# Performance work log

Measured on AMD Instinct MI355X. Metric: run time of the kernel, lower is better.

## Reference

```python
import jax, jax.numpy as jnp
import numpy as np

# --- constants (structural / non-tensor args of run()) ---
B = 1024        # number of independent systems (replicas)
NDOF = 64       # degrees of freedom per system (x0.shape[-1])
N_CHAIN = 2     # thermostat chain length
DT = 0.002      # integration time step
N_STEPS = 200   # number of MD steps


def force_fn(x):
    # harmonic potential U = 0.5*|x|^2  ->  F = -x
    return -x


def setup_inputs() -> dict:
    key = jax.random.key(0)
    k1, k2 = jax.random.split(key)
    x0 = jax.random.normal(k1, (B, NDOF), dtype=jnp.float32)
    v0 = jax.random.normal(k2, (B, NDOF), dtype=jnp.float32)
    kT = jnp.ones((), dtype=jnp.float32)
    mass = jnp.ones((), dtype=jnp.float32)
    Q = jnp.ones((), dtype=jnp.float32)
    return {"x0": x0, "v0": v0, "kT": kT, "mass": mass, "Q": Q}


def _nhc_step(x, v, xi, kT, mass, Q):
    dt = DT
    ndof = NDOF
    # xi: (..., N_CHAIN)
    KE = 0.5 * mass * jnp.sum(v * v, axis=-1)            # (...,)
    G = (2.0 * KE - ndof * kT) / Q
    xi_list = [xi[..., j] for j in range(N_CHAIN)]
    # first half chain update, j = n_chain-1 .. 0 (staggered half steps)
    for j in range(N_CHAIN - 1, -1, -1):
        if j == N_CHAIN - 1:
            xi_list[j] = xi_list[j] + dt / 4 * G
        else:
            s = jnp.exp(-xi_list[j + 1] * dt / 8)
            xi_list[j] = (xi_list[j] * s + dt / 4 * G) * s
        if j == 0:
            v = v * jnp.exp(-xi_list[0][..., None] * dt / 2)
            KE = 0.5 * mass * jnp.sum(v * v, axis=-1)
        G = (2.0 * KE - ndof * kT) / Q if j == 0 else (Q * xi_list[j - 1] ** 2 - kT) / Q
    # velocity-Verlet inner step
    v = v + dt / 2 * force_fn(x) / mass
    x = x + dt * v
    v = v + dt / 2 * force_fn(x) / mass
    KE = 0.5 * mass * jnp.sum(v * v, axis=-1)
    G = (2.0 * KE - ndof * kT) / Q
    # second half chain update, j = 0 .. n_chain-1
    for j in range(N_CHAIN):
        if j == 0:
            v = v * jnp.exp(-xi_list[0][..., None] * dt / 2)
            KE = 0.5 * mass * jnp.sum(v * v, axis=-1)
            G = (2.0 * KE - ndof * kT) / Q
        if j == N_CHAIN - 1:
            xi_list[j] = xi_list[j] + dt / 4 * G
        else:
            s = jnp.exp(-xi_list[j + 1] * dt / 8)
            xi_list[j] = (xi_list[j] * s + dt / 4 * G) * s
        G = (Q * xi_list[j] ** 2 - kT) / Q
    return x, v, jnp.stack(xi_list, axis=-1)


def _run(x0, v0, kT, mass, Q):
    xi0 = jnp.zeros(x0.shape[:-1] + (N_CHAIN,), dtype=x0.dtype)

    def body(carry, _):
        x, v, xi = carry
        x, v, xi = _nhc_step(x, v, xi, kT, mass, Q)
        return (x, v, xi), (x, v)

    _, (xs, vs) = jax.lax.scan(body, (x0, v0, xi0), xs=None, length=N_STEPS)
    traj_x = jnp.concatenate([x0[None], xs], axis=0)   # (N_STEPS+1, B, NDOF)
    traj_v = jnp.concatenate([v0[None], vs], axis=0)
    return traj_x, traj_v


def reference(x0, v0, kT, mass, Q):
    return _run(x0, v0, kT, mass, Q)
```

## Files before the change

### kernel.cpp

```cpp
#include <hip/hip_runtime.h>

#define NB     1024
#define NDOF   64
#define NSTEPS 200
#define DTF    0.002f

__global__ __launch_bounds__(256) void nhc_kernel(
    const float* __restrict__ x0, const float* __restrict__ v0,
    const float* __restrict__ kTp, const float* __restrict__ massp,
    const float* __restrict__ Qp, float* __restrict__ out)
{
    const int tid  = blockIdx.x * blockDim.x + threadIdx.x;
    const int sys  = tid >> 6;
    const int lane = tid & 63;
    if (sys >= NB) return;

    const float kT   = kTp[0];
    const float mass = massp[0];
    const float Q    = Qp[0];

    const float dt   = DTF;
    const float dt2  = 0.5f   * DTF;
    const float dt4  = 0.25f  * DTF;
    const float dt8  = 0.125f * DTF;
    const float invQ = 1.0f / Q;
    const float mi   = mass * invQ;
    const float c    = dt2 / mass;
    const float alpha = 1.0f - dt * c;

    const float K1 = c * c * (alpha + 1.0f) * (alpha + 1.0f);
    const float K2 = 2.0f * dt * c * c * (alpha + 2.0f) - 4.0f * c;
    const float K3 = alpha * alpha;
    const float A1 = alpha * alpha, A2 = 2.0f * dt * alpha, A3 = dt * dt;
    const float L1 = -c * alpha * (alpha + 1.0f);
    const float L2 = 1.0f - 2.0f * dt * c * (alpha + 1.0f);
    const float L3 = dt * alpha;
    const float Bs = -dt8, As = 0.5f * dt8 * dt8;
    const float Bc = -dt2, Ac = 0.5f * dt2 * dt2;
    const float Bu = -dt,  Au = 0.5f * dt * dt;
    const float negC   = -(float)NDOF * kT * invQ;
    const float negkTQ = -kT * invQ;

    float x = x0[sys * NDOF + lane];
    float v = v0[sys * NDOF + lane];

    float* __restrict__ out_x = out;
    float* __restrict__ out_v = out + (size_t)(NSTEPS + 1) * NB * NDOF;

    out_x[sys * NDOF + lane] = x;
    out_v[sys * NDOF + lane] = v;

    float sxx = x * x, sxv = x * v, svv = v * v;
    #pragma unroll
    for (int off = 32; off; off >>= 1) {
        sxx += __shfl_xor(sxx, off, 64);
        sxv += __shfl_xor(sxv, off, 64);
        svv += __shfl_xor(svv, off, 64);
    }
    float Sxx = mi * sxx, Sxv = mi * sxv, Svv = mi * svv;
    float P1 = K1 * Sxx, P2 = K2 * Sxv, P3 = K3 * Svv;

    float xi0 = 0.0f;
    float xi1 = dt4 * (Svv + negC);
    float t0  = dt4 * negkTQ;

    size_t widx = (size_t)NB * NDOF + sys * NDOF + lane;

    for (int n = 0; n < NSTEPS; ++n) {
        float s  = fmaf(xi1, fmaf(As, xi1, Bs), 1.0f);
        xi0 = fmaf(xi0, s, t0) * s;
        float sc = fmaf(xi0, fmaf(Ac, xi0, Bc), 1.0f);
        float u  = fmaf(xi0, fmaf(Au, xi0, Bu), 1.0f);
        float b  = fmaf(u, P3, fmaf(sc, P2, P1));
        float Gt = fmaf(u, b, negC);
        float t  = dt4 * Gt;
        xi0 = fmaf(xi0, s, t) * s;
        float G1 = fmaf(xi0, xi0, negkTQ);
        xi1 = xi1 + fmaf(dt4, G1, t);
        t0  = dt4 * G1;

        float X = sc * Sxv, V = u * Svv;
        float Sxx1 = fmaf(A1, Sxx, fmaf(A2, X, A3 * V));
        Sxv = sc * fmaf(L1, Sxx, fmaf(L2, X, L3 * V));
        Svv = u * b;
        Sxx = Sxx1;
        P1 = K1 * Sxx; P2 = K2 * Sxv; P3 = K3 * Svv;

        v *= sc;
        v = fmaf(-c, x, v);
        x = fmaf(dt, v, x);
        v = fmaf(-c, x, v);
        v *= sc;

        out_x[widx] = x;
        out_v[widx] = v;
        widx += (size_t)NB * NDOF;
    }
}

extern "C" void kernel_launch(void* const* d_in, const int* in_sizes, int n_in,
                              void* d_out, int out_size, void* d_ws, size_t ws_size,
                              hipStream_t stream) {
    const float* x0   = (const float*)d_in[0];
    const float* v0   = (const float*)d_in[1];
    const float* kT   = (const float*)d_in[2];
    const float* mass = (const float*)d_in[3];
    const float* Q    = (const float*)d_in[4];
    float* out = (float*)d_out;

    const int total = NB * NDOF;
    const int block = 256;
    const int grid  = total / block;
    nhc_kernel<<<grid, block, 0, stream>>>(x0, v0, kT, mass, Q, out);
}
```

Before: 122.2 us.

## Split NHC integration into per-step propagator scan and parallel trajectory expansion

Phase 1 runs the serial thermostat recurrence per system and accumulates a 2x2 linear propagator matrix per step, storing one float4 per (system, step) in workspace. Phase 2 launches one thread per float4 of output across all steps and computes x,v directly from x0,v0 and that matrix, giving fully parallel, vectorised, coalesced trajectory writes. The aim is to break the serial 200-step store chain of the original kernel into a bandwidth-bound parallel write. It adds a second launch, a workspace round trip, and a fallback fused kernel, and it may change rounding relative to stepwise integration.

```diff
diff --git a/kernel.cpp b/kernel.cpp
--- a/kernel.cpp
+++ b/kernel.cpp
@@ -5,10 +5,10 @@
 #define NSTEPS 200
 #define DTF    0.002f
 
-__global__ __launch_bounds__(256) void nhc_kernel(
+__global__ __launch_bounds__(256) void nhc_phase1(
     const float* __restrict__ x0, const float* __restrict__ v0,
     const float* __restrict__ kTp, const float* __restrict__ massp,
-    const float* __restrict__ Qp, float* __restrict__ out)
+    const float* __restrict__ Qp, float4* __restrict__ P)
 {
     const int tid  = blockIdx.x * blockDim.x + threadIdx.x;
     const int sys  = tid >> 6;
@@ -27,6 +27,7 @@
     const float mi   = mass * invQ;
     const float c    = dt2 / mass;
     const float alpha = 1.0f - dt * c;
+    const float gamma = -c * (2.0f - dt * c);
 
     const float K1 = c * c * (alpha + 1.0f) * (alpha + 1.0f);
     const float K2 = 2.0f * dt * c * c * (alpha + 2.0f) - 4.0f * c;
@@ -41,14 +42,8 @@
     const float negC   = -(float)NDOF * kT * invQ;
     const float negkTQ = -kT * invQ;
 
-    float x = x0[sys * NDOF + lane];
-    float v = v0[sys * NDOF + lane];
-
-    float* __restrict__ out_x = out;
-    float* __restrict__ out_v = out + (size_t)(NSTEPS + 1) * NB * NDOF;
-
-    out_x[sys * NDOF + lane] = x;
-    out_v[sys * NDOF + lane] = v;
+    const float x = x0[sys * NDOF + lane];
+    const float v = v0[sys * NDOF + lane];
 
     float sxx = x * x, sxv = x * v, svv = v * v;
     #pragma unroll
@@ -64,7 +59,8 @@
     float xi1 = dt4 * (Svv + negC);
     float t0  = dt4 * negkTQ;
 
-    size_t widx = (size_t)NB * NDOF + sys * NDOF + lane;
+    float p00 = 1.0f, p01 = 0.0f, p10 = 0.0f, p11 = 1.0f;
+    float k0 = 0.0f, k1 = 0.0f, k2 = 0.0f, k3 = 0.0f;
 
     for (int n = 0; n < NSTEPS; ++n) {
         float s  = fmaf(xi1, fmaf(As, xi1, Bs), 1.0f);
@@ -86,15 +82,130 @@
         Sxx = Sxx1;
         P1 = K1 * Sxx; P2 = K2 * Sxv; P3 = K3 * Svv;
 
-        v *= sc;
-        v = fmaf(-c, x, v);
-        x = fmaf(dt, v, x);
-        v = fmaf(-c, x, v);
-        v *= sc;
-
-        out_x[widx] = x;
-        out_v[widx] = v;
-        widx += (size_t)NB * NDOF;
+        float bb = dt * sc, g = gamma * sc, a2 = alpha * u;
+        float q00 = fmaf(alpha, p00, bb * p10);
+        float q01 = fmaf(alpha, p01, bb * p11);
+        float q10 = fmaf(g,     p00, a2 * p10);
+        float q11 = fmaf(g,     p01, a2 * p11);
+        p00 = q00; p01 = q01; p10 = q10; p11 = q11;
+
+        const bool sel = (lane == (n & 63));
+        k0 = sel ? p00 : k0;
+        k1 = sel ? p01 : k1;
+        k2 = sel ? p10 : k2;
+        k3 = sel ? p11 : k3;
+
+        if ((n & 63) == 63) {
+            P[sys * NSTEPS + (n - 63) + lane] = make_float4(k0, k1, k2, k3);
+        }
+    }
+    if (lane < (NSTEPS & 63)) {
+        P[sys * NSTEPS + (NSTEPS & ~63) + lane] = make_float4(k0, k1, k2, k3);
+    }
+}
+
+#define F4_PER_SYS  (NDOF / 4)
+#define F4_PER_STEP (NB * F4_PER_SYS)
+#define TOTAL_F4    ((NSTEPS + 1) * F4_PER_STEP)
+
+__global__ __launch_bounds__(256) void nhc_phase2(
+    const float* __restrict__ x0, const float* __restrict__ v0,
+    const float4* __restrict__ P, float* __restrict__ out)
+{
+    const int t = blockIdx.x * blockDim.x + threadIdx.x;
+    if (t >= TOTAL_F4) return;
+
+    const int step = t >> 14;
+    const int rem  = t & (F4_PER_STEP - 1);
+    const int sys  = rem >> 4;
+    const int q    = rem & 15;
+
+    const float4 xv = *reinterpret_cast<const float4*>(&x0[sys * NDOF + q * 4]);
+    const float4 vv = *reinterpret_cast<const float4*>(&v0[sys * NDOF + q * 4]);
+
+    const size_t o = (size_t)step * (NB * NDOF) + sys * NDOF + q * 4;
+    float4* __restrict__ ox = reinterpret_cast<float4*>(&out[o]);
+    float4* __restrict__ ov = reinterpret_cast<float4*>(
+        &out[o + (size_t)(NSTEPS + 1) * NB * NDOF]);
+
+    if (step == 0) {
+        *ox = xv;
+        *ov = vv;
+        return;
+    }
+    const float4 p = P[sys * NSTEPS + (step - 1)];
+    float4 rx, rv;
+    rx.x = fmaf(p.x, xv.x, p.y * vv.x);  rv.x = fmaf(p.z, xv.x, p.w * vv.x);
+    rx.y = fmaf(p.x, xv.y, p.y * vv.y);  rv.y = fmaf(p.z, xv.y, p.w * vv.y);
+    rx.z = fmaf(p.x, xv.z, p.y * vv.z);  rv.z = fmaf(p.z, xv.z, p.w * vv.z);
+    rx.w = fmaf(p.x, xv.w, p.y * vv.w);  rv.w = fmaf(p.z, xv.w, p.w * vv.w);
+    *ox = rx;
+    *ov = rv;
+}
+
+__global__ __launch_bounds__(256) void nhc_fused(
+    const float* __restrict__ x0, const float* __restrict__ v0,
+    const float* __restrict__ kTp, const float* __restrict__ massp,
+    const float* __restrict__ Qp, float* __restrict__ out)
+{
+    const int tid  = blockIdx.x * blockDim.x + threadIdx.x;
+    const int sys  = tid >> 6;
+    const int lane = tid & 63;
+    if (sys >= NB) return;
+
+    const float kT = kTp[0], mass = massp[0], Q = Qp[0];
+    const float dt = DTF, dt2 = 0.5f*DTF, dt4 = 0.25f*DTF, dt8 = 0.125f*DTF;
+    const float invQ = 1.0f/Q, mi = mass*invQ, c = dt2/mass;
+    const float alpha = 1.0f - dt*c;
+    const float K1 = c*c*(alpha+1.0f)*(alpha+1.0f);
+    const float K2 = 2.0f*dt*c*c*(alpha+2.0f) - 4.0f*c;
+    const float K3 = alpha*alpha;
+    const float A1 = alpha*alpha, A2 = 2.0f*dt*alpha, A3 = dt*dt;
+    const float L1 = -c*alpha*(alpha+1.0f);
+    const float L2 = 1.0f - 2.0f*dt*c*(alpha+1.0f);
+    const float L3 = dt*alpha;
+    const float Bs = -dt8, As = 0.5f*dt8*dt8;
+    const float Bc = -dt2, Ac = 0.5f*dt2*dt2;
+    const float Bu = -dt,  Au = 0.5f*dt*dt;
+    const float negC = -(float)NDOF*kT*invQ, negkTQ = -kT*invQ;
+
+    float x = x0[sys*NDOF+lane], v = v0[sys*NDOF+lane];
+    float* __restrict__ out_x = out;
+    float* __restrict__ out_v = out + (size_t)(NSTEPS+1)*NB*NDOF;
+    out_x[sys*NDOF+lane] = x;  out_v[sys*NDOF+lane] = v;
+
+    float sxx = x*x, sxv = x*v, svv = v*v;
+    #pragma unroll
+    for (int off = 32; off; off >>= 1) {
+        sxx += __shfl_xor(sxx, off, 64);
+        sxv += __shfl_xor(sxv, off, 64);
+        svv += __shfl_xor(svv, off, 64);
+    }
+    float Sxx = mi*sxx, Sxv = mi*sxv, Svv = mi*svv;
+    float P1 = K1*Sxx, P2 = K2*Sxv, P3 = K3*Svv;
+    float xi0 = 0.0f, xi1 = dt4*(Svv+negC), t0 = dt4*negkTQ;
+    size_t widx = (size_t)NB*NDOF + sys*NDOF + lane;
+
+    for (int n = 0; n < NSTEPS; ++n) {
+        float s  = fmaf(xi1, fmaf(As, xi1, Bs), 1.0f);
+        xi0 = fmaf(xi0, s, t0) * s;
+        float sc = fmaf(xi0, fmaf(Ac, xi0, Bc), 1.0f);
+        float u  = fmaf(xi0, fmaf(Au, xi0, Bu), 1.0f);
+        float b  = fmaf(u, P3, fmaf(sc, P2, P1));
+        float Gt = fmaf(u, b, negC);
+        float t  = dt4 * Gt;
+        xi0 = fmaf(xi0, s, t) * s;
+        float G1 = fmaf(xi0, xi0, negkTQ);
+        xi1 = xi1 + fmaf(dt4, G1, t);
+        t0  = dt4 * G1;
+        float X = sc*Sxv, V = u*Svv;
+        float Sxx1 = fmaf(A1, Sxx, fmaf(A2, X, A3*V));
+        Sxv = sc*fmaf(L1, Sxx, fmaf(L2, X, L3*V));
+        Svv = u*b;  Sxx = Sxx1;
+        P1 = K1*Sxx; P2 = K2*Sxv; P3 = K3*Svv;
+        v *= sc;  v = fmaf(-c,x,v);  x = fmaf(dt,v,x);  v = fmaf(-c,x,v);  v *= sc;
+        out_x[widx] = x;  out_v[widx] = v;
+        widx += (size_t)NB*NDOF;
     }
 }
 
@@ -108,8 +219,15 @@
     const float* Q    = (const float*)d_in[4];
     float* out = (float*)d_out;
 
-    const int total = NB * NDOF;
-    const int block = 256;
-    const int grid  = total / block;
-    nhc_kernel<<<grid, block, 0, stream>>>(x0, v0, kT, mass, Q, out);
-}
+    const size_t ws_needed = (size_t)NB * NSTEPS * 4 * sizeof(float);
+    if (ws_size < ws_needed) {
+        nhc_fused<<<NB * NDOF / 256, 256, 0, stream>>>(x0, v0, kT, mass, Q, out);
+        return;
+    }
+    float4* P = (float4*)d_ws;
+
+    nhc_phase1<<<NB * NDOF / 256, 256, 0, stream>>>(x0, v0, kT, mass, Q, P);
+
+    const int blocks = TOTAL_F4 / 256;
+    nhc_phase2<<<blocks, 256, 0, stream>>>(x0, v0, P, out);
+}
```

Measured after the change: 139.8 us. +14.5%, slower.
